# Optimization experiments

Measured on AMD Instinct MI355X. Metric: run time of the kernel, lower is better.

## Reference

```python
import jax, jax.numpy as jnp
import numpy as np

B, U, L, H, M = 4, 16, 128, 768, 256   # docs, utterances/doc, tokens/utt, hidden, mentions/doc
HID = 150                               # Score MLP hidden dim
N_CLUSTERS = 32


def setup_inputs() -> dict:
    key = jax.random.key(0)
    ks = jax.random.split(key, 8)
    hidden = jax.random.normal(ks[0], (B, U, L, H), jnp.float32)

    rng = np.random.default_rng(0)
    span_utt = rng.integers(0, U, (B, M))
    span_start = rng.integers(0, L - 8, (B, M))
    span_end = span_start + rng.integers(1, 9, (B, M))  # span length in [1, 8]

    # coreference labels: label[i, j] = 1 iff j is a true antecedent (j < i, same cluster);
    # if mention i has no antecedent, label[i, i] = 1 (the epsilon / new-entity slot).
    clusters = rng.integers(0, N_CLUSTERS, (B, M))
    same = clusters[:, :, None] == clusters[:, None, :]
    ant = same & np.tril(np.ones((M, M), bool), -1)
    labels = ant.astype(np.float32)
    diag = np.arange(M)
    labels[:, diag, diag] = (~ant.any(-1)).astype(np.float32)

    scale = 0.02
    W1 = jax.random.normal(ks[1], (3 * H, HID), jnp.float32) * scale
    W2 = jax.random.normal(ks[2], (HID, HID), jnp.float32) * scale
    W3 = jax.random.normal(ks[3], (HID, 1), jnp.float32) * scale
    return {
        "hidden": hidden,
        "span_utt": jnp.asarray(span_utt, jnp.int32),
        "span_start": jnp.asarray(span_start, jnp.int32),
        "span_end": jnp.asarray(span_end, jnp.int32),
        "labels": jnp.asarray(labels),
        "W1": W1, "b1": jnp.zeros((HID,), jnp.float32),
        "W2": W2, "b2": jnp.zeros((HID,), jnp.float32),
        "W3": W3, "b3": jnp.zeros((1,), jnp.float32),
    }


def reference(hidden, span_utt, span_start, span_end, labels, W1, b1, W2, b2, W3, b3):
    # ---- span mean-pooling (EntityEncoder, aggr='mean') ----
    pos = jnp.arange(L)
    mask = (pos[None, None, :] >= span_start[..., None]) & (pos[None, None, :] < span_end[..., None])
    w = mask.astype(hidden.dtype) / (span_end - span_start)[..., None].astype(hidden.dtype)  # [B,M,L]
    gathered = jnp.take_along_axis(hidden, span_utt[:, :, None, None], axis=1)  # [B,M,L,H]
    pooled = jnp.einsum('bml,bmlh->bmh', w, gathered)  # [B,M,H]

    # ---- pairwise antecedent scoring (PairScorer / Score MLP, dropout=eval) ----
    ii, jj = np.tril_indices(M, -1)  # static pair indices, P = M(M-1)/2
    # concat(i_g, j_g, i_g*j_g) @ W1  ==  i_g@W1a + j_g@W1b + (i_g*j_g)@W1c
    W1a, W1b, W1c = W1[:H], W1[H:2 * H], W1[2 * H:]
    hi = pooled @ W1a   # [B,M,HID]
    hj = pooled @ W1b   # [B,M,HID]
    prod = pooled[:, ii] * pooled[:, jj]                    # [B,P,H]
    h1 = jax.nn.relu(hi[:, ii] + hj[:, jj] + prod @ W1c + b1)
    h2 = jax.nn.relu(h1 @ W2 + b2)
    s = (h2 @ W3 + b3)[..., 0]  # [B,P]

    # ---- per-mention ragged softmax, padded to [M, M] with -1000 ----
    # row i has logits s_ij for j<i plus epsilon=0 at j=i (diagonal of zeros matrix)
    logits = jnp.zeros((B, M, M), hidden.dtype).at[:, ii, jj].set(s)
    valid = jnp.tril(jnp.ones((M, M), bool))
    probs = jax.nn.softmax(jnp.where(valid, logits, -1e30), axis=-1)
    probs = jnp.where(valid, probs, jnp.asarray(-1000.0, hidden.dtype))

    # ---- compute_loss ----
    eps = 1e-8
    prob_sum = jnp.sum(jnp.clip(probs * labels, eps, 1.0 - eps), axis=-1)  # [B,M]
    loss = -jnp.sum(jnp.log(prob_sum))
    return loss
```

## Files before the change

kernel.cpp:

```cpp
#include <hip/hip_runtime.h>
#include <hip/hip_bf16.h>

#define B_ 4
#define U_ 16
#define L_ 128
#define H_ 768
#define M_ 256
#define HID_ 150

typedef _Float16 half8 __attribute__((ext_vector_type(8)));
typedef _Float16 half4t __attribute__((ext_vector_type(4)));
typedef float floatx4 __attribute__((ext_vector_type(4)));
typedef float floatx16 __attribute__((ext_vector_type(16)));

__device__ __forceinline__ void gl_lds16(const _Float16* g, _Float16* l)
{
    __builtin_amdgcn_global_load_lds(
        (const __attribute__((address_space(1))) unsigned int*)g,
        (__attribute__((address_space(3))) unsigned int*)l, 16, 0, 0);
}

__global__ __launch_bounds__(256) void prep_kernel(
    const float* __restrict__ W1, const float* __restrict__ W2,
    const float* __restrict__ b2, const float* __restrict__ W3,
    _Float16* __restrict__ W1cs, _Float16* __restrict__ W2s,
    _Float16* __restrict__ W1abs, float2* __restrict__ bw)
{
    int idx = blockIdx.x * 256 + threadIdx.x;
    if (blockIdx.x == 0 && threadIdx.x < 160) {
        int n = threadIdx.x;
        bw[n] = (n < HID_) ? make_float2(b2[n], W3[n]) : make_float2(0.f, 0.f);
    }
    if (idx < 122880) {
        int k = idx / 160, n = idx - k * 160;
        float v = (n < HID_) ? W1[(size_t)(2 * H_ + k) * HID_ + n] : 0.f;
        W1cs[(k >> 4) * 2560 + (n >> 5) * 512 +
             (((n & 31) | (((k >> 3) & 1) << 5)) << 3) + (k & 7)] = (_Float16)v;
        return;
    }
    idx -= 122880;
    if (idx < 25600) {
        int k = idx / 160, n = idx - k * 160;
        float v = (k < HID_ && n < HID_) ? W2[(size_t)k * HID_ + n] : 0.f;
        W2s[(k >> 4) * 2560 + (n >> 5) * 512 +
            (((n & 31) | (((k >> 3) & 1) << 5)) << 3) + (k & 7)] = (_Float16)v;
        return;
    }
    idx -= 25600;
    if (idx < 245760) {
        int k = idx / 320, n = idx - k * 320;
        float v = 0.f;
        if (n < HID_) v = W1[(size_t)k * HID_ + n];
        else if (n >= 160 && n < 160 + HID_) v = W1[(size_t)(H_ + k) * HID_ + (n - 160)];
        W1abs[(k >> 5) * 10240 + (n >> 4) * 512 +
              (((n & 15) | (((k >> 3) & 3) << 4)) << 3) + (k & 7)] = (_Float16)v;
    }
}

__global__ __launch_bounds__(256) void pool_kernel(
    const float* __restrict__ hidden, const int* __restrict__ sutt,
    const int* __restrict__ sstart, const int* __restrict__ send,
    _Float16* __restrict__ pooledh)
{
    const int bm = blockIdx.x * 4 + (threadIdx.x >> 6);
    const int lane = threadIdx.x & 63;
    const int b  = bm >> 8;
    const int u  = sutt[bm];
    const int st = sstart[bm];
    const int en = send[bm];
    const float inv = 1.0f / (float)(en - st);
    const float* src = hidden + ((size_t)(b * U_ + u) * L_) * H_ + lane * 12;
    float4 s[3];
    #pragma unroll
    for (int q = 0; q < 3; ++q) s[q] = make_float4(0.f, 0.f, 0.f, 0.f);
    for (int l = st; l < en; ++l) {
        const float* p = src + (size_t)l * H_;
        #pragma unroll
        for (int q = 0; q < 3; ++q) {
            float4 v = *(const float4*)(p + q * 4);
            s[q].x += v.x; s[q].y += v.y; s[q].z += v.z; s[q].w += v.w;
        }
    }
    _Float16* gp = pooledh + (size_t)bm * H_ + lane * 12;
    #pragma unroll
    for (int q = 0; q < 3; ++q) {
        half4t hv;
        hv[0] = (_Float16)(s[q].x * inv); hv[1] = (_Float16)(s[q].y * inv);
        hv[2] = (_Float16)(s[q].z * inv); hv[3] = (_Float16)(s[q].w * inv);
        *(half4t*)(gp + q * 4) = hv;
    }
}

__global__ __launch_bounds__(256) void hihj_kernel(
    const _Float16* __restrict__ pooledh, const float* __restrict__ b1,
    const _Float16* __restrict__ W1abs,
    float* __restrict__ hiF, float* __restrict__ hjT)
{
    __shared__ __align__(16) _Float16 spool[16 * 776];
    const int blk = blockIdx.x;
    const int tid = threadIdx.x;
    for (int e = tid; e < 16 * 96; e += 256) {
        int r = e / 96, c = e - r * 96;
        *(half8*)&spool[r * 776 + c * 8] =
            *(const half8*)&pooledh[(size_t)(blk * 16 + r) * H_ + c * 8];
    }
    __syncthreads();

    const int w = tid >> 6, lane = tid & 63;
    const int g = lane >> 4, l15 = lane & 15;
    floatx4 acc[5];
    #pragma unroll
    for (int u5 = 0; u5 < 5; ++u5) acc[u5] = (floatx4){0.f, 0.f, 0.f, 0.f};
    const _Float16* aB = &spool[l15 * 776 + g * 8];
    for (int kc = 0; kc < 24; ++kc) {
        half8 av = *(const half8*)(aB + kc * 32);
        #pragma unroll
        for (int u5 = 0; u5 < 5; ++u5) {
            const int u = w * 5 + u5;
            half8 bv = *(const half8*)(W1abs + (size_t)((kc * 20 + u) * 64 + lane) * 8);
            acc[u5] = __builtin_amdgcn_mfma_f32_16x16x32_f16(av, bv, acc[u5], 0, 0, 0);
        }
    }
    const int row0 = blk * 16 + g * 4;
    #pragma unroll
    for (int u5 = 0; u5 < 5; ++u5) {
        const int n = (w * 5 + u5) * 16 + l15;
        if (n < HID_) {
            float b1v = b1[n];
            #pragma unroll
            for (int r = 0; r < 4; ++r)
                hiF[(size_t)(row0 + r) * 160 + n] = acc[u5][r] + b1v;
        } else if (n >= 160 && n < 160 + HID_) {
            *(float4*)&hjT[(size_t)(n - 160) * 1024 + row0] =
                make_float4(acc[u5][0], acc[u5][1], acc[u5][2], acc[u5][3]);
        }
    }
}

__global__ __launch_bounds__(128, 2) void pair_mlp_kernel(
    const _Float16* __restrict__ pooledh,
    const float* __restrict__ hiF, const float* __restrict__ hjT,
    const _Float16* __restrict__ W1cs, const _Float16* __restrict__ W2s,
    const float2* __restrict__ bw, const float* __restrict__ b3,
    float* __restrict__ logits)
{
    __shared__ __align__(16) _Float16 smem[2 * 5440];

    int q = blockIdx.x;
    const int b = q / 576;
    int r = q - b * 576;
    int jt = 0;
    while (r >= 128 - 16 * jt) { r -= 128 - 16 * jt; ++jt; }
    const int p = 16 * jt + r;
    const int i0 = 2 * p, j0 = jt * 32;
    const int bm = b * M_;
    const int w = threadIdx.x >> 6;
    const int lane = threadIdx.x & 63;
    const int c31 = lane & 31;
    const int hw = lane >> 5;

    _Float16* Wb0 = smem;
    _Float16* Wb1 = smem + 5120;
    _Float16* h1w = smem + w * 5440;

    const _Float16* pjp = pooledh + (size_t)(bm + j0 + c31) * H_ + (hw << 3);
    const _Float16* pip = pooledh + (size_t)(bm + i0 + w) * H_ + (hw << 3);

    floatx16 acc1[5];
    #pragma unroll
    for (int t1 = 0; t1 < 5; ++t1)
        #pragma unroll
        for (int e = 0; e < 16; ++e) acc1[t1][e] = 0.f;

    {
        const _Float16* gW = W1cs + (size_t)(5 * w) * 512 + lane * 8;
        #pragma unroll
        for (int c = 0; c < 5; ++c)
            gl_lds16(gW + c * 512, Wb0 + (5 * w + c) * 512);
    }
    half8 Apj0 = *(const half8*)(pjp);
    half8 Apj1 = *(const half8*)(pjp + 16);
    half8 Ai0  = *(const half8*)(pip);
    half8 Ai1  = *(const half8*)(pip + 16);
    __syncthreads();

    for (int kc = 0; kc < 24; ++kc) {
        const _Float16* Wcur = (kc & 1) ? Wb1 : Wb0;
        _Float16*       Wnxt = (kc & 1) ? Wb0 : Wb1;
        half8 npj0, npj1, ni0, ni1;
        if (kc < 23) {
            const _Float16* gW = W1cs + (size_t)(kc + 1) * 5120 + (5 * w) * 512 + lane * 8;
            #pragma unroll
            for (int c = 0; c < 5; ++c)
                gl_lds16(gW + c * 512, Wnxt + (5 * w + c) * 512);
            const int kb = (kc + 1) * 32;
            npj0 = *(const half8*)(pjp + kb);
            npj1 = *(const half8*)(pjp + kb + 16);
            ni0  = *(const half8*)(pip + kb);
            ni1  = *(const half8*)(pip + kb + 16);
        }
        {
            half8 a = Ai0 * Apj0;
            #pragma unroll
            for (int t1 = 0; t1 < 5; ++t1) {
                half8 wf = *(const half8*)&Wcur[t1 * 512 + lane * 8];
                acc1[t1] = __builtin_amdgcn_mfma_f32_32x32x16_f16(wf, a, acc1[t1], 0, 0, 0);
            }
        }
        {
            half8 a = Ai1 * Apj1;
            #pragma unroll
            for (int t1 = 0; t1 < 5; ++t1) {
                half8 wf = *(const half8*)&Wcur[(5 + t1) * 512 + lane * 8];
                acc1[t1] = __builtin_amdgcn_mfma_f32_32x32x16_f16(wf, a, acc1[t1], 0, 0, 0);
            }
        }
        if (kc < 23) { Apj0 = npj0; Apj1 = npj1; Ai0 = ni0; Ai1 = ni1; }
        __syncthreads();
    }

    const int jcol = bm + j0 + c31;
    #pragma unroll
    for (int t1 = 0; t1 < 5; ++t1) {
        #pragma unroll
        for (int qd = 0; qd < 4; ++qd) {
            const int n1 = t1 * 32 + 8 * qd + 4 * hw;
            float hj0 = hjT[(size_t)(n1 + 0) * 1024 + jcol];
            float hj1 = hjT[(size_t)(n1 + 1) * 1024 + jcol];
            float hj2 = hjT[(size_t)(n1 + 2) * 1024 + jcol];
            float hj3 = hjT[(size_t)(n1 + 3) * 1024 + jcol];
            float4 hiv = *(const float4*)&hiF[(size_t)(bm + i0 + w) * 160 + n1];
            half4t hv;
            hv[0] = (_Float16)fmaxf(acc1[t1][4 * qd + 0] + hiv.x + hj0, 0.f);
            hv[1] = (_Float16)fmaxf(acc1[t1][4 * qd + 1] + hiv.y + hj1, 0.f);
            hv[2] = (_Float16)fmaxf(acc1[t1][4 * qd + 2] + hiv.z + hj2, 0.f);
            hv[3] = (_Float16)fmaxf(acc1[t1][4 * qd + 3] + hiv.w + hj3, 0.f);
            *(half4t*)&h1w[c31 * 170 + n1] = hv;
        }
    }
    __syncthreads();

    const float b3v = b3[0];
    floatx16 acc2[5];
    #pragma unroll
    for (int t2 = 0; t2 < 5; ++t2)
        #pragma unroll
        for (int e = 0; e < 16; ++e) acc2[t2][e] = 0.f;

    half8 W2b[2][5], h1b[2];
    #pragma unroll
    for (int c = 0; c < 2; ++c) {
        const _Float16* wb = W2s + (size_t)(c * 5) * 512 + lane * 8;
        #pragma unroll
        for (int t2 = 0; t2 < 5; ++t2) W2b[c][t2] = *(const half8*)(wb + t2 * 512);
        h1b[c] = *(const half8*)&h1w[c31 * 170 + c * 16 + hw * 8];
    }
    for (int kc2 = 0; kc2 < 10; ++kc2) {
        const int cur = kc2 & 1;
        half8 nw[5], nh;
        if (kc2 < 8) {
            const _Float16* wb = W2s + (size_t)((kc2 + 2) * 5) * 512 + lane * 8;
            #pragma unroll
            for (int t2 = 0; t2 < 5; ++t2) nw[t2] = *(const half8*)(wb + t2 * 512);
            nh = *(const half8*)&h1w[c31 * 170 + (kc2 + 2) * 16 + hw * 8];
        }
        #pragma unroll
        for (int t2 = 0; t2 < 5; ++t2)
            acc2[t2] = __builtin_amdgcn_mfma_f32_32x32x16_f16(
                W2b[cur][t2], h1b[cur], acc2[t2], 0, 0, 0);
        if (kc2 < 8) {
            #pragma unroll
            for (int t2 = 0; t2 < 5; ++t2) W2b[cur][t2] = nw[t2];
            h1b[cur] = nh;
        }
    }

    float sown = 0.f;
    #pragma unroll
    for (int t2 = 0; t2 < 5; ++t2) {
        #pragma unroll
        for (int qd = 0; qd < 4; ++qd) {
            const int n2 = t2 * 32 + 8 * qd + 4 * hw;
            float4 bw01 = *(const float4*)&bw[n2];
            float4 bw23 = *(const float4*)&bw[n2 + 2];
            sown += fmaxf(acc2[t2][4 * qd + 0] + bw01.x, 0.f) * bw01.y;
            sown += fmaxf(acc2[t2][4 * qd + 1] + bw01.z, 0.f) * bw01.w;
            sown += fmaxf(acc2[t2][4 * qd + 2] + bw23.x, 0.f) * bw23.y;
            sown += fmaxf(acc2[t2][4 * qd + 3] + bw23.z, 0.f) * bw23.w;
        }
    }
    float s = sown + __shfl_xor(sown, 32);
    const int i = i0 + w;
    const int j = j0 + c31;
    if (lane < 32 && j < i)
        logits[(size_t)(bm + i) * M_ + j] = s + b3v;
}

__global__ __launch_bounds__(256) void loss_kernel(
    const float* __restrict__ logits, const float* __restrict__ labels,
    float* __restrict__ out)
{
    const int bm = blockIdx.x;
    const int i  = bm & (M_ - 1);
    const int j  = threadIdx.x;
    __shared__ float red[4];
    __shared__ float bcast;

    float val = (j < i) ? logits[(size_t)bm * M_ + j]
                        : ((j == i) ? 0.0f : -1e30f);

    float m = val;
    #pragma unroll
    for (int off = 32; off >= 1; off >>= 1) m = fmaxf(m, __shfl_down(m, off, 64));
    const int wave = j >> 6, lane = j & 63;
    if (lane == 0) red[wave] = m;
    __syncthreads();
    if (j == 0) bcast = fmaxf(fmaxf(red[0], red[1]), fmaxf(red[2], red[3]));
    __syncthreads();
    const float mm = bcast;

    float e = (j <= i) ? expf(val - mm) : 0.0f;
    float s = e;
    #pragma unroll
    for (int off = 32; off >= 1; off >>= 1) s += __shfl_down(s, off, 64);
    __syncthreads();
    if (lane == 0) red[wave] = s;
    __syncthreads();
    if (j == 0) bcast = red[0] + red[1] + red[2] + red[3];
    __syncthreads();
    const float ssum = bcast;

    float prob = (j <= i) ? (e / ssum) : -1000.0f;
    float lab = labels[(size_t)bm * M_ + j];
    float tv = prob * lab;
    tv = fminf(fmaxf(tv, 1e-8f), 1.0f - 1e-8f);
    float rs = tv;
    #pragma unroll
    for (int off = 32; off >= 1; off >>= 1) rs += __shfl_down(rs, off, 64);
    __syncthreads();
    if (lane == 0) red[wave] = rs;
    __syncthreads();
    if (j == 0) atomicAdd(out, -logf(red[0] + red[1] + red[2] + red[3]));
}

extern "C" void kernel_launch(void* const* d_in, const int* in_sizes, int n_in,
                              void* d_out, int out_size, void* d_ws, size_t ws_size,
                              hipStream_t stream)
{
    const float* hidden = (const float*)d_in[0];
    const int*   sutt   = (const int*)d_in[1];
    const int*   sstart = (const int*)d_in[2];
    const int*   send   = (const int*)d_in[3];
    const float* labels = (const float*)d_in[4];
    const float* W1     = (const float*)d_in[5];
    const float* b1     = (const float*)d_in[6];
    const float* W2     = (const float*)d_in[7];
    const float* b2     = (const float*)d_in[8];
    const float* W3     = (const float*)d_in[9];
    const float* b3     = (const float*)d_in[10];

    float* ws = (float*)d_ws;
    float*    hiF     = ws;
    float*    hjT     = ws + 163840;
    float*    logits  = ws + 327680;
    float2*   bw      = (float2*)(ws + 589824);
    _Float16* pooledh = (_Float16*)(ws + 590144);
    _Float16* W1cs    = (_Float16*)(ws + 983360);
    _Float16* W2s     = (_Float16*)(ws + 1106240);
    _Float16* W1abs   = (_Float16*)(ws + 1119040);
    float* out = (float*)d_out;

    hipMemsetAsync(d_out, 0, sizeof(float), stream);

    prep_kernel<<<dim3(1540), 256, 0, stream>>>(W1, W2, b2, W3,
                                                W1cs, W2s, W1abs, bw);
    pool_kernel<<<dim3(256), 256, 0, stream>>>(hidden, sutt, sstart, send, pooledh);
    hihj_kernel<<<dim3(64), 256, 0, stream>>>(pooledh, b1, W1abs, hiF, hjT);
    pair_mlp_kernel<<<dim3(576 * B_), 128, 0, stream>>>(pooledh, hiF, hjT,
                                                        W1cs, W2s, bw, b3, logits);
    loss_kernel<<<dim3(B_ * M_), 256, 0, stream>>>(logits, labels, out);
}
```

Measured before the change: 202.2 us.

## Use single-wave pair MLP blocks with register-prefetched W1c, fuse prep and pool

The pair MLP kernel goes from 2-wave blocks that staged W1c tiles through LDS with global_load_lds and a barrier per k-chunk to 1-wave blocks (twice as many). Each wave loads its W1c fragments straight from global into registers, double-buffered two chunks ahead, so the per-iteration __syncthreads goes away. Separately, the pooling kernel is merged into the weight-prep kernel as extra blocks, saving one launch. The trade-off is higher register pressure (20 half8 weight fragments plus the accumulators) and that each wave now reads the full W1c on its own instead of sharing it through LDS.

```diff
diff --git a/kernel.cpp b/kernel.cpp
--- a/kernel.cpp
+++ b/kernel.cpp
@@ -13,19 +13,45 @@
 typedef float floatx4 __attribute__((ext_vector_type(4)));
 typedef float floatx16 __attribute__((ext_vector_type(16)));
 
-__device__ __forceinline__ void gl_lds16(const _Float16* g, _Float16* l)
-{
-    __builtin_amdgcn_global_load_lds(
-        (const __attribute__((address_space(1))) unsigned int*)g,
-        (__attribute__((address_space(3))) unsigned int*)l, 16, 0, 0);
-}
-
-__global__ __launch_bounds__(256) void prep_kernel(
+__global__ __launch_bounds__(256) void prep_pool_kernel(
     const float* __restrict__ W1, const float* __restrict__ W2,
     const float* __restrict__ b2, const float* __restrict__ W3,
+    const float* __restrict__ hidden, const int* __restrict__ sutt,
+    const int* __restrict__ sstart, const int* __restrict__ send,
     _Float16* __restrict__ W1cs, _Float16* __restrict__ W2s,
-    _Float16* __restrict__ W1abs, float2* __restrict__ bw)
-{
+    _Float16* __restrict__ W1abs, float2* __restrict__ bw,
+    _Float16* __restrict__ pooledh)
+{
+    if (blockIdx.x >= 1540) {
+        const int bm = (blockIdx.x - 1540) * 4 + (threadIdx.x >> 6);
+        const int lane = threadIdx.x & 63;
+        const int b  = bm >> 8;
+        const int u  = sutt[bm];
+        const int st = sstart[bm];
+        const int en = send[bm];
+        const float inv = 1.0f / (float)(en - st);
+        const float* src = hidden + ((size_t)(b * U_ + u) * L_) * H_ + lane * 12;
+        float4 s[3];
+        #pragma unroll
+        for (int q = 0; q < 3; ++q) s[q] = make_float4(0.f, 0.f, 0.f, 0.f);
+        for (int l = st; l < en; ++l) {
+            const float* p = src + (size_t)l * H_;
+            #pragma unroll
+            for (int q = 0; q < 3; ++q) {
+                float4 v = *(const float4*)(p + q * 4);
+                s[q].x += v.x; s[q].y += v.y; s[q].z += v.z; s[q].w += v.w;
+            }
+        }
+        _Float16* gp = pooledh + (size_t)bm * H_ + lane * 12;
+        #pragma unroll
+        for (int q = 0; q < 3; ++q) {
+            half4t hv;
+            hv[0] = (_Float16)(s[q].x * inv); hv[1] = (_Float16)(s[q].y * inv);
+            hv[2] = (_Float16)(s[q].z * inv); hv[3] = (_Float16)(s[q].w * inv);
+            *(half4t*)(gp + q * 4) = hv;
+        }
+        return;
+    }
     int idx = blockIdx.x * 256 + threadIdx.x;
     if (blockIdx.x == 0 && threadIdx.x < 160) {
         int n = threadIdx.x;
@@ -57,40 +83,6 @@
     }
 }
 
-__global__ __launch_bounds__(256) void pool_kernel(
-    const float* __restrict__ hidden, const int* __restrict__ sutt,
-    const int* __restrict__ sstart, const int* __restrict__ send,
-    _Float16* __restrict__ pooledh)
-{
-    const int bm = blockIdx.x * 4 + (threadIdx.x >> 6);
-    const int lane = threadIdx.x & 63;
-    const int b  = bm >> 8;
-    const int u  = sutt[bm];
-    const int st = sstart[bm];
-    const int en = send[bm];
-    const float inv = 1.0f / (float)(en - st);
-    const float* src = hidden + ((size_t)(b * U_ + u) * L_) * H_ + lane * 12;
-    float4 s[3];
-    #pragma unroll
-    for (int q = 0; q < 3; ++q) s[q] = make_float4(0.f, 0.f, 0.f, 0.f);
-    for (int l = st; l < en; ++l) {
-        const float* p = src + (size_t)l * H_;
-        #pragma unroll
-        for (int q = 0; q < 3; ++q) {
-            float4 v = *(const float4*)(p + q * 4);
-            s[q].x += v.x; s[q].y += v.y; s[q].z += v.z; s[q].w += v.w;
-        }
-    }
-    _Float16* gp = pooledh + (size_t)bm * H_ + lane * 12;
-    #pragma unroll
-    for (int q = 0; q < 3; ++q) {
-        half4t hv;
-        hv[0] = (_Float16)(s[q].x * inv); hv[1] = (_Float16)(s[q].y * inv);
-        hv[2] = (_Float16)(s[q].z * inv); hv[3] = (_Float16)(s[q].w * inv);
-        *(half4t*)(gp + q * 4) = hv;
-    }
-}
-
 __global__ __launch_bounds__(256) void hihj_kernel(
     const _Float16* __restrict__ pooledh, const float* __restrict__ b1,
     const _Float16* __restrict__ W1abs,
@@ -137,34 +129,31 @@
     }
 }
 
-__global__ __launch_bounds__(128, 2) void pair_mlp_kernel(
+__global__ __launch_bounds__(64, 2) void pair_mlp_kernel(
     const _Float16* __restrict__ pooledh,
     const float* __restrict__ hiF, const float* __restrict__ hjT,
     const _Float16* __restrict__ W1cs, const _Float16* __restrict__ W2s,
     const float2* __restrict__ bw, const float* __restrict__ b3,
     float* __restrict__ logits)
 {
-    __shared__ __align__(16) _Float16 smem[2 * 5440];
+    __shared__ __align__(16) _Float16 h1L[32 * 170];
 
     int q = blockIdx.x;
-    const int b = q / 576;
-    int r = q - b * 576;
+    const int b = q / 1152;
+    int r2 = q - b * 1152;
+    const int t = r2 & 1;
+    int r = r2 >> 1;
     int jt = 0;
     while (r >= 128 - 16 * jt) { r -= 128 - 16 * jt; ++jt; }
     const int p = 16 * jt + r;
-    const int i0 = 2 * p, j0 = jt * 32;
+    const int i = 2 * p + t, j0 = jt * 32;
     const int bm = b * M_;
-    const int w = threadIdx.x >> 6;
     const int lane = threadIdx.x & 63;
     const int c31 = lane & 31;
     const int hw = lane >> 5;
 
-    _Float16* Wb0 = smem;
-    _Float16* Wb1 = smem + 5120;
-    _Float16* h1w = smem + w * 5440;
-
     const _Float16* pjp = pooledh + (size_t)(bm + j0 + c31) * H_ + (hw << 3);
-    const _Float16* pip = pooledh + (size_t)(bm + i0 + w) * H_ + (hw << 3);
+    const _Float16* pip = pooledh + (size_t)(bm + i) * H_ + (hw << 3);
 
     floatx16 acc1[5];
     #pragma unroll
@@ -172,51 +161,53 @@
         #pragma unroll
         for (int e = 0; e < 16; ++e) acc1[t1][e] = 0.f;
 
-    {
-        const _Float16* gW = W1cs + (size_t)(5 * w) * 512 + lane * 8;
-        #pragma unroll
-        for (int c = 0; c < 5; ++c)
-            gl_lds16(gW + c * 512, Wb0 + (5 * w + c) * 512);
-    }
-    half8 Apj0 = *(const half8*)(pjp);
-    half8 Apj1 = *(const half8*)(pjp + 16);
-    half8 Ai0  = *(const half8*)(pip);
-    half8 Ai1  = *(const half8*)(pip + 16);
-    __syncthreads();
+    half8 Apj0[2], Apj1[2], Ai0[2], Ai1[2];
+    half8 Wf[2][10];
+    #pragma unroll
+    for (int c = 0; c < 2; ++c) {
+        const int kb = c * 32;
+        Apj0[c] = *(const half8*)(pjp + kb);
+        Apj1[c] = *(const half8*)(pjp + kb + 16);
+        Ai0[c]  = *(const half8*)(pip + kb);
+        Ai1[c]  = *(const half8*)(pip + kb + 16);
+        const _Float16* wb = W1cs + (size_t)c * 5120 + lane * 8;
+        #pragma unroll
+        for (int u = 0; u < 10; ++u) Wf[c][u] = *(const half8*)(wb + u * 512);
+    }
 
     for (int kc = 0; kc < 24; ++kc) {
-        const _Float16* Wcur = (kc & 1) ? Wb1 : Wb0;
-        _Float16*       Wnxt = (kc & 1) ? Wb0 : Wb1;
-        half8 npj0, npj1, ni0, ni1;
-        if (kc < 23) {
-            const _Float16* gW = W1cs + (size_t)(kc + 1) * 5120 + (5 * w) * 512 + lane * 8;
-            #pragma unroll
-            for (int c = 0; c < 5; ++c)
-                gl_lds16(gW + c * 512, Wnxt + (5 * w + c) * 512);
-            const int kb = (kc + 1) * 32;
+        const int cur = kc & 1;
+        half8 npj0, npj1, ni0, ni1, nW[10];
+        if (kc < 22) {
+            const int kb = (kc + 2) * 32;
             npj0 = *(const half8*)(pjp + kb);
             npj1 = *(const half8*)(pjp + kb + 16);
             ni0  = *(const half8*)(pip + kb);
             ni1  = *(const half8*)(pip + kb + 16);
+            const _Float16* wb = W1cs + (size_t)(kc + 2) * 5120 + lane * 8;
+            #pragma unroll
+            for (int u = 0; u < 10; ++u) nW[u] = *(const half8*)(wb + u * 512);
         }
         {
-            half8 a = Ai0 * Apj0;
-            #pragma unroll
-            for (int t1 = 0; t1 < 5; ++t1) {
-                half8 wf = *(const half8*)&Wcur[t1 * 512 + lane * 8];
-                acc1[t1] = __builtin_amdgcn_mfma_f32_32x32x16_f16(wf, a, acc1[t1], 0, 0, 0);
-            }
+            half8 a = Ai0[cur] * Apj0[cur];
+            #pragma unroll
+            for (int t1 = 0; t1 < 5; ++t1)
+                acc1[t1] = __builtin_amdgcn_mfma_f32_32x32x16_f16(
+                    Wf[cur][t1], a, acc1[t1], 0, 0, 0);
         }
         {
-            half8 a = Ai1 * Apj1;
-            #pragma unroll
-            for (int t1 = 0; t1 < 5; ++t1) {
-                half8 wf = *(const half8*)&Wcur[(5 + t1) * 512 + lane * 8];
-                acc1[t1] = __builtin_amdgcn_mfma_f32_32x32x16_f16(wf, a, acc1[t1], 0, 0, 0);
-            }
-        }
-        if (kc < 23) { Apj0 = npj0; Apj1 = npj1; Ai0 = ni0; Ai1 = ni1; }
-        __syncthreads();
+            half8 a = Ai1[cur] * Apj1[cur];
+            #pragma unroll
+            for (int t1 = 0; t1 < 5; ++t1)
+                acc1[t1] = __builtin_amdgcn_mfma_f32_32x32x16_f16(
+                    Wf[cur][5 + t1], a, acc1[t1], 0, 0, 0);
+        }
+        if (kc < 22) {
+            Apj0[cur] = npj0; Apj1[cur] = npj1;
+            Ai0[cur] = ni0;   Ai1[cur] = ni1;
+            #pragma unroll
+            for (int u = 0; u < 10; ++u) Wf[cur][u] = nW[u];
+        }
     }
 
     const int jcol = bm + j0 + c31;
@@ -229,13 +220,13 @@
             float hj1 = hjT[(size_t)(n1 + 1) * 1024 + jcol];
             float hj2 = hjT[(size_t)(n1 + 2) * 1024 + jcol];
             float hj3 = hjT[(size_t)(n1 + 3) * 1024 + jcol];
-            float4 hiv = *(const float4*)&hiF[(size_t)(bm + i0 + w) * 160 + n1];
+            float4 hiv = *(const float4*)&hiF[(size_t)(bm + i) * 160 + n1];
             half4t hv;
             hv[0] = (_Float16)fmaxf(acc1[t1][4 * qd + 0] + hiv.x + hj0, 0.f);
             hv[1] = (_Float16)fmaxf(acc1[t1][4 * qd + 1] + hiv.y + hj1, 0.f);
             hv[2] = (_Float16)fmaxf(acc1[t1][4 * qd + 2] + hiv.z + hj2, 0.f);
             hv[3] = (_Float16)fmaxf(acc1[t1][4 * qd + 3] + hiv.w + hj3, 0.f);
-            *(half4t*)&h1w[c31 * 170 + n1] = hv;
+            *(half4t*)&h1L[c31 * 170 + n1] = hv;
         }
     }
     __syncthreads();
@@ -253,7 +244,7 @@
         const _Float16* wb = W2s + (size_t)(c * 5) * 512 + lane * 8;
         #pragma unroll
         for (int t2 = 0; t2 < 5; ++t2) W2b[c][t2] = *(const half8*)(wb + t2 * 512);
-        h1b[c] = *(const half8*)&h1w[c31 * 170 + c * 16 + hw * 8];
+        h1b[c] = *(const half8*)&h1L[c31 * 170 + c * 16 + hw * 8];
     }
     for (int kc2 = 0; kc2 < 10; ++kc2) {
         const int cur = kc2 & 1;
@@ -262,7 +253,7 @@
             const _Float16* wb = W2s + (size_t)((kc2 + 2) * 5) * 512 + lane * 8;
             #pragma unroll
             for (int t2 = 0; t2 < 5; ++t2) nw[t2] = *(const half8*)(wb + t2 * 512);
-            nh = *(const half8*)&h1w[c31 * 170 + (kc2 + 2) * 16 + hw * 8];
+            nh = *(const half8*)&h1L[c31 * 170 + (kc2 + 2) * 16 + hw * 8];
         }
         #pragma unroll
         for (int t2 = 0; t2 < 5; ++t2)
@@ -290,7 +281,6 @@
         }
     }
     float s = sown + __shfl_xor(sown, 32);
-    const int i = i0 + w;
     const int j = j0 + c31;
     if (lane < 32 && j < i)
         logits[(size_t)(bm + i) * M_ + j] = s + b3v;
@@ -372,11 +362,11 @@
 
     hipMemsetAsync(d_out, 0, sizeof(float), stream);
 
-    prep_kernel<<<dim3(1540), 256, 0, stream>>>(W1, W2, b2, W3,
-                                                W1cs, W2s, W1abs, bw);
-    pool_kernel<<<dim3(256), 256, 0, stream>>>(hidden, sutt, sstart, send, pooledh);
+    prep_pool_kernel<<<dim3(1796), 256, 0, stream>>>(
+        W1, W2, b2, W3, hidden, sutt, sstart, send,
+        W1cs, W2s, W1abs, bw, pooledh);
     hihj_kernel<<<dim3(64), 256, 0, stream>>>(pooledh, b1, W1abs, hiF, hjT);
-    pair_mlp_kernel<<<dim3(576 * B_), 128, 0, stream>>>(pooledh, hiF, hjT,
+    pair_mlp_kernel<<<dim3(1152 * B_), 64, 0, stream>>>(pooledh, hiF, hjT,
                                                         W1cs, W2s, bw, b3, logits);
     loss_kernel<<<dim3(B_ * M_), 256, 0, stream>>>(logits, labels, out);
 }
```

Result: slower. 234.7 us (+16.1%).

## Merge weight prep with span pooling and double K-chunk per W1c pipeline stage

Applied to the files above, without the earlier changes.

The weight-reformatting kernel and the span mean-pooling kernel become one launch: extra blocks past index 1540 do the pooling, which removes a launch and lets the two independent jobs overlap. In the pair MLP kernel, each double-buffered stage now loads two 32-wide K chunks of W1c (64 K values) into LDS instead of one. That halves the loop iterations and __syncthreads barriers from 24 to 12. The cost is twice the LDS footprint (about 40KB), which may reduce occupancy, plus more registers for the prefetched operands.

```diff
diff --git a/kernel.cpp b/kernel.cpp
--- a/kernel.cpp
+++ b/kernel.cpp
@@ -20,12 +20,45 @@
         (__attribute__((address_space(3))) unsigned int*)l, 16, 0, 0);
 }
 
-__global__ __launch_bounds__(256) void prep_kernel(
+__global__ __launch_bounds__(256) void prep_pool_kernel(
     const float* __restrict__ W1, const float* __restrict__ W2,
     const float* __restrict__ b2, const float* __restrict__ W3,
+    const float* __restrict__ hidden, const int* __restrict__ sutt,
+    const int* __restrict__ sstart, const int* __restrict__ send,
     _Float16* __restrict__ W1cs, _Float16* __restrict__ W2s,
-    _Float16* __restrict__ W1abs, float2* __restrict__ bw)
-{
+    _Float16* __restrict__ W1abs, float2* __restrict__ bw,
+    _Float16* __restrict__ pooledh)
+{
+    if (blockIdx.x >= 1540) {
+        const int bm = (blockIdx.x - 1540) * 4 + (threadIdx.x >> 6);
+        const int lane = threadIdx.x & 63;
+        const int b  = bm >> 8;
+        const int u  = sutt[bm];
+        const int st = sstart[bm];
+        const int en = send[bm];
+        const float inv = 1.0f / (float)(en - st);
+        const float* src = hidden + ((size_t)(b * U_ + u) * L_) * H_ + lane * 12;
+        float4 s[3];
+        #pragma unroll
+        for (int q = 0; q < 3; ++q) s[q] = make_float4(0.f, 0.f, 0.f, 0.f);
+        for (int l = st; l < en; ++l) {
+            const float* p = src + (size_t)l * H_;
+            #pragma unroll
+            for (int q = 0; q < 3; ++q) {
+                float4 v = *(const float4*)(p + q * 4);
+                s[q].x += v.x; s[q].y += v.y; s[q].z += v.z; s[q].w += v.w;
+            }
+        }
+        _Float16* gp = pooledh + (size_t)bm * H_ + lane * 12;
+        #pragma unroll
+        for (int q = 0; q < 3; ++q) {
+            half4t hv;
+            hv[0] = (_Float16)(s[q].x * inv); hv[1] = (_Float16)(s[q].y * inv);
+            hv[2] = (_Float16)(s[q].z * inv); hv[3] = (_Float16)(s[q].w * inv);
+            *(half4t*)(gp + q * 4) = hv;
+        }
+        return;
+    }
     int idx = blockIdx.x * 256 + threadIdx.x;
     if (blockIdx.x == 0 && threadIdx.x < 160) {
         int n = threadIdx.x;
@@ -57,40 +90,6 @@
     }
 }
 
-__global__ __launch_bounds__(256) void pool_kernel(
-    const float* __restrict__ hidden, const int* __restrict__ sutt,
-    const int* __restrict__ sstart, const int* __restrict__ send,
-    _Float16* __restrict__ pooledh)
-{
-    const int bm = blockIdx.x * 4 + (threadIdx.x >> 6);
-    const int lane = threadIdx.x & 63;
-    const int b  = bm >> 8;
-    const int u  = sutt[bm];
-    const int st = sstart[bm];
-    const int en = send[bm];
-    const float inv = 1.0f / (float)(en - st);
-    const float* src = hidden + ((size_t)(b * U_ + u) * L_) * H_ + lane * 12;
-    float4 s[3];
-    #pragma unroll
-    for (int q = 0; q < 3; ++q) s[q] = make_float4(0.f, 0.f, 0.f, 0.f);
-    for (int l = st; l < en; ++l) {
-        const float* p = src + (size_t)l * H_;
-        #pragma unroll
-        for (int q = 0; q < 3; ++q) {
-            float4 v = *(const float4*)(p + q * 4);
-            s[q].x += v.x; s[q].y += v.y; s[q].z += v.z; s[q].w += v.w;
-        }
-    }
-    _Float16* gp = pooledh + (size_t)bm * H_ + lane * 12;
-    #pragma unroll
-    for (int q = 0; q < 3; ++q) {
-        half4t hv;
-        hv[0] = (_Float16)(s[q].x * inv); hv[1] = (_Float16)(s[q].y * inv);
-        hv[2] = (_Float16)(s[q].z * inv); hv[3] = (_Float16)(s[q].w * inv);
-        *(half4t*)(gp + q * 4) = hv;
-    }
-}
-
 __global__ __launch_bounds__(256) void hihj_kernel(
     const _Float16* __restrict__ pooledh, const float* __restrict__ b1,
     const _Float16* __restrict__ W1abs,
@@ -144,7 +143,7 @@
     const float2* __restrict__ bw, const float* __restrict__ b3,
     float* __restrict__ logits)
 {
-    __shared__ __align__(16) _Float16 smem[2 * 5440];
+    __shared__ __align__(16) _Float16 smem[2 * 10240];
 
     int q = blockIdx.x;
     const int b = q / 576;
@@ -160,7 +159,7 @@
     const int hw = lane >> 5;
 
     _Float16* Wb0 = smem;
-    _Float16* Wb1 = smem + 5120;
+    _Float16* Wb1 = smem + 10240;
     _Float16* h1w = smem + w * 5440;
 
     const _Float16* pjp = pooledh + (size_t)(bm + j0 + c31) * H_ + (hw << 3);
@@ -175,47 +174,74 @@
     {
         const _Float16* gW = W1cs + (size_t)(5 * w) * 512 + lane * 8;
         #pragma unroll
-        for (int c = 0; c < 5; ++c)
-            gl_lds16(gW + c * 512, Wb0 + (5 * w + c) * 512);
-    }
-    half8 Apj0 = *(const half8*)(pjp);
-    half8 Apj1 = *(const half8*)(pjp + 16);
-    half8 Ai0  = *(const half8*)(pip);
-    half8 Ai1  = *(const half8*)(pip + 16);
-    __syncthreads();
-
-    for (int kc = 0; kc < 24; ++kc) {
-        const _Float16* Wcur = (kc & 1) ? Wb1 : Wb0;
-        _Float16*       Wnxt = (kc & 1) ? Wb0 : Wb1;
-        half8 npj0, npj1, ni0, ni1;
-        if (kc < 23) {
-            const _Float16* gW = W1cs + (size_t)(kc + 1) * 5120 + (5 * w) * 512 + lane * 8;
+        for (int cc = 0; cc < 2; ++cc)
             #pragma unroll
             for (int c = 0; c < 5; ++c)
-                gl_lds16(gW + c * 512, Wnxt + (5 * w + c) * 512);
-            const int kb = (kc + 1) * 32;
-            npj0 = *(const half8*)(pjp + kb);
-            npj1 = *(const half8*)(pjp + kb + 16);
-            ni0  = *(const half8*)(pip + kb);
-            ni1  = *(const half8*)(pip + kb + 16);
-        }
-        {
-            half8 a = Ai0 * Apj0;
-            #pragma unroll
-            for (int t1 = 0; t1 < 5; ++t1) {
-                half8 wf = *(const half8*)&Wcur[t1 * 512 + lane * 8];
-                acc1[t1] = __builtin_amdgcn_mfma_f32_32x32x16_f16(wf, a, acc1[t1], 0, 0, 0);
+                gl_lds16(gW + cc * 5120 + c * 512,
+                         Wb0 + cc * 5120 + (5 * w + c) * 512);
+    }
+    half8 Apj0[2], Apj1[2], Ai0[2], Ai1[2];
+    #pragma unroll
+    for (int cc = 0; cc < 2; ++cc) {
+        const int kb = cc * 32;
+        Apj0[cc] = *(const half8*)(pjp + kb);
+        Apj1[cc] = *(const half8*)(pjp + kb + 16);
+        Ai0[cc]  = *(const half8*)(pip + kb);
+        Ai1[cc]  = *(const half8*)(pip + kb + 16);
+    }
+    __syncthreads();
+
+    for (int kt = 0; kt < 12; ++kt) {
+        const _Float16* Wcur = (kt & 1) ? Wb1 : Wb0;
+        _Float16*       Wnxt = (kt & 1) ? Wb0 : Wb1;
+        half8 npj0[2], npj1[2], ni0[2], ni1[2];
+        if (kt < 11) {
+            const _Float16* gW = W1cs + (size_t)(kt + 1) * 10240
+                                 + (5 * w) * 512 + lane * 8;
+            #pragma unroll
+            for (int cc = 0; cc < 2; ++cc)
+                #pragma unroll
+                for (int c = 0; c < 5; ++c)
+                    gl_lds16(gW + cc * 5120 + c * 512,
+                             Wnxt + cc * 5120 + (5 * w + c) * 512);
+            const int kb = (kt + 1) * 64;
+            #pragma unroll
+            for (int cc = 0; cc < 2; ++cc) {
+                npj0[cc] = *(const half8*)(pjp + kb + cc * 32);
+                npj1[cc] = *(const half8*)(pjp + kb + cc * 32 + 16);
+                ni0[cc]  = *(const half8*)(pip + kb + cc * 32);
+                ni1[cc]  = *(const half8*)(pip + kb + cc * 32 + 16);
             }
         }
-        {
-            half8 a = Ai1 * Apj1;
-            #pragma unroll
-            for (int t1 = 0; t1 < 5; ++t1) {
-                half8 wf = *(const half8*)&Wcur[(5 + t1) * 512 + lane * 8];
-                acc1[t1] = __builtin_amdgcn_mfma_f32_32x32x16_f16(wf, a, acc1[t1], 0, 0, 0);
+        #pragma unroll
+        for (int cc = 0; cc < 2; ++cc) {
+            const _Float16* Wc = Wcur + cc * 5120;
+            {
+                half8 a = Ai0[cc] * Apj0[cc];
+                #pragma unroll
+                for (int t1 = 0; t1 < 5; ++t1) {
+                    half8 wf = *(const half8*)&Wc[t1 * 512 + lane * 8];
+                    acc1[t1] = __builtin_amdgcn_mfma_f32_32x32x16_f16(
+                        wf, a, acc1[t1], 0, 0, 0);
+                }
             }
-        }
-        if (kc < 23) { Apj0 = npj0; Apj1 = npj1; Ai0 = ni0; Ai1 = ni1; }
+            {
+                half8 a = Ai1[cc] * Apj1[cc];
+                #pragma unroll
+                for (int t1 = 0; t1 < 5; ++t1) {
+                    half8 wf = *(const half8*)&Wc[(5 + t1) * 512 + lane * 8];
+                    acc1[t1] = __builtin_amdgcn_mfma_f32_32x32x16_f16(
+                        wf, a, acc1[t1], 0, 0, 0);
+                }
+            }
+        }
+        if (kt < 11) {
+            #pragma unroll
+            for (int cc = 0; cc < 2; ++cc) {
+                Apj0[cc] = npj0[cc]; Apj1[cc] = npj1[cc];
+                Ai0[cc]  = ni0[cc];  Ai1[cc]  = ni1[cc];
+            }
+        }
         __syncthreads();
     }
 
@@ -372,9 +398,9 @@
 
     hipMemsetAsync(d_out, 0, sizeof(float), stream);
 
-    prep_kernel<<<dim3(1540), 256, 0, stream>>>(W1, W2, b2, W3,
-                                                W1cs, W2s, W1abs, bw);
-    pool_kernel<<<dim3(256), 256, 0, stream>>>(hidden, sutt, sstart, send, pooledh);
+    prep_pool_kernel<<<dim3(1796), 256, 0, stream>>>(
+        W1, W2, b2, W3, hidden, sutt, sstart, send,
+        W1cs, W2s, W1abs, bw, pooledh);
     hihj_kernel<<<dim3(64), 256, 0, stream>>>(pooledh, b1, W1abs, hiF, hjT);
     pair_mlp_kernel<<<dim3(576 * B_), 128, 0, stream>>>(pooledh, hiF, hjT,
                                                         W1cs, W2s, bw, b3, logits);
```

Result: slower. 206.3 us (+2.0%).

## Process four i-rows per pair block and merge prep with pooling kernel

Applied to the files above, without the earlier changes.

The pair MLP kernel now has each wave handle two i-rows instead of one. Every W1c tile staged in LDS and every pooled j-fragment load therefore feeds two MFMAs, which halves the grid and the per-row weight traffic. The weight-prep and span-pooling kernels are merged into one launch by giving pooling its own block range. The cost is twice the layer-1 accumulator registers per wave, which may lower occupancy under the 128,2 launch bounds, plus a serialized layer-2 pass per row.

```diff
diff --git a/kernel.cpp b/kernel.cpp
--- a/kernel.cpp
+++ b/kernel.cpp
@@ -20,12 +20,45 @@
         (__attribute__((address_space(3))) unsigned int*)l, 16, 0, 0);
 }
 
-__global__ __launch_bounds__(256) void prep_kernel(
+__global__ __launch_bounds__(256) void prep_pool_kernel(
     const float* __restrict__ W1, const float* __restrict__ W2,
     const float* __restrict__ b2, const float* __restrict__ W3,
+    const float* __restrict__ hidden, const int* __restrict__ sutt,
+    const int* __restrict__ sstart, const int* __restrict__ send,
     _Float16* __restrict__ W1cs, _Float16* __restrict__ W2s,
-    _Float16* __restrict__ W1abs, float2* __restrict__ bw)
-{
+    _Float16* __restrict__ W1abs, float2* __restrict__ bw,
+    _Float16* __restrict__ pooledh)
+{
+    if (blockIdx.x >= 1540) {
+        const int bm = (blockIdx.x - 1540) * 4 + (threadIdx.x >> 6);
+        const int lane = threadIdx.x & 63;
+        const int b  = bm >> 8;
+        const int u  = sutt[bm];
+        const int st = sstart[bm];
+        const int en = send[bm];
+        const float inv = 1.0f / (float)(en - st);
+        const float* src = hidden + ((size_t)(b * U_ + u) * L_) * H_ + lane * 12;
+        float4 s[3];
+        #pragma unroll
+        for (int q = 0; q < 3; ++q) s[q] = make_float4(0.f, 0.f, 0.f, 0.f);
+        for (int l = st; l < en; ++l) {
+            const float* p = src + (size_t)l * H_;
+            #pragma unroll
+            for (int q = 0; q < 3; ++q) {
+                float4 v = *(const float4*)(p + q * 4);
+                s[q].x += v.x; s[q].y += v.y; s[q].z += v.z; s[q].w += v.w;
+            }
+        }
+        _Float16* gp = pooledh + (size_t)bm * H_ + lane * 12;
+        #pragma unroll
+        for (int q = 0; q < 3; ++q) {
+            half4t hv;
+            hv[0] = (_Float16)(s[q].x * inv); hv[1] = (_Float16)(s[q].y * inv);
+            hv[2] = (_Float16)(s[q].z * inv); hv[3] = (_Float16)(s[q].w * inv);
+            *(half4t*)(gp + q * 4) = hv;
+        }
+        return;
+    }
     int idx = blockIdx.x * 256 + threadIdx.x;
     if (blockIdx.x == 0 && threadIdx.x < 160) {
         int n = threadIdx.x;
@@ -57,40 +90,6 @@
     }
 }
 
-__global__ __launch_bounds__(256) void pool_kernel(
-    const float* __restrict__ hidden, const int* __restrict__ sutt,
-    const int* __restrict__ sstart, const int* __restrict__ send,
-    _Float16* __restrict__ pooledh)
-{
-    const int bm = blockIdx.x * 4 + (threadIdx.x >> 6);
-    const int lane = threadIdx.x & 63;
-    const int b  = bm >> 8;
-    const int u  = sutt[bm];
-    const int st = sstart[bm];
-    const int en = send[bm];
-    const float inv = 1.0f / (float)(en - st);
-    const float* src = hidden + ((size_t)(b * U_ + u) * L_) * H_ + lane * 12;
-    float4 s[3];
-    #pragma unroll
-    for (int q = 0; q < 3; ++q) s[q] = make_float4(0.f, 0.f, 0.f, 0.f);
-    for (int l = st; l < en; ++l) {
-        const float* p = src + (size_t)l * H_;
-        #pragma unroll
-        for (int q = 0; q < 3; ++q) {
-            float4 v = *(const float4*)(p + q * 4);
-            s[q].x += v.x; s[q].y += v.y; s[q].z += v.z; s[q].w += v.w;
-        }
-    }
-    _Float16* gp = pooledh + (size_t)bm * H_ + lane * 12;
-    #pragma unroll
-    for (int q = 0; q < 3; ++q) {
-        half4t hv;
-        hv[0] = (_Float16)(s[q].x * inv); hv[1] = (_Float16)(s[q].y * inv);
-        hv[2] = (_Float16)(s[q].z * inv); hv[3] = (_Float16)(s[q].w * inv);
-        *(half4t*)(gp + q * 4) = hv;
-    }
-}
-
 __global__ __launch_bounds__(256) void hihj_kernel(
     const _Float16* __restrict__ pooledh, const float* __restrict__ b1,
     const _Float16* __restrict__ W1abs,
@@ -147,12 +146,12 @@
     __shared__ __align__(16) _Float16 smem[2 * 5440];
 
     int q = blockIdx.x;
-    const int b = q / 576;
-    int r = q - b * 576;
+    const int b = q / 288;
+    int r = q - b * 288;
     int jt = 0;
-    while (r >= 128 - 16 * jt) { r -= 128 - 16 * jt; ++jt; }
-    const int p = 16 * jt + r;
-    const int i0 = 2 * p, j0 = jt * 32;
+    while (r >= 64 - 8 * jt) { r -= 64 - 8 * jt; ++jt; }
+    const int p4 = 8 * jt + r;
+    const int i0 = 4 * p4, j0 = jt * 32;
     const int bm = b * M_;
     const int w = threadIdx.x >> 6;
     const int lane = threadIdx.x & 63;
@@ -163,14 +162,18 @@
     _Float16* Wb1 = smem + 5120;
     _Float16* h1w = smem + w * 5440;
 
-    const _Float16* pjp = pooledh + (size_t)(bm + j0 + c31) * H_ + (hw << 3);
-    const _Float16* pip = pooledh + (size_t)(bm + i0 + w) * H_ + (hw << 3);
-
-    floatx16 acc1[5];
-    #pragma unroll
-    for (int t1 = 0; t1 < 5; ++t1)
-        #pragma unroll
-        for (int e = 0; e < 16; ++e) acc1[t1][e] = 0.f;
+    const int ia = i0 + 2 * w;
+    const _Float16* pjp  = pooledh + (size_t)(bm + j0 + c31) * H_ + (hw << 3);
+    const _Float16* pipa = pooledh + (size_t)(bm + ia) * H_ + (hw << 3);
+    const _Float16* pipb = pooledh + (size_t)(bm + ia + 1) * H_ + (hw << 3);
+
+    floatx16 acc1[2][5];
+    #pragma unroll
+    for (int t = 0; t < 2; ++t)
+        #pragma unroll
+        for (int t1 = 0; t1 < 5; ++t1)
+            #pragma unroll
+            for (int e = 0; e < 16; ++e) acc1[t][t1][e] = 0.f;
 
     {
         const _Float16* gW = W1cs + (size_t)(5 * w) * 512 + lane * 8;
@@ -180,14 +183,16 @@
     }
     half8 Apj0 = *(const half8*)(pjp);
     half8 Apj1 = *(const half8*)(pjp + 16);
-    half8 Ai0  = *(const half8*)(pip);
-    half8 Ai1  = *(const half8*)(pip + 16);
+    half8 Aa0  = *(const half8*)(pipa);
+    half8 Aa1  = *(const half8*)(pipa + 16);
+    half8 Ab0  = *(const half8*)(pipb);
+    half8 Ab1  = *(const half8*)(pipb + 16);
     __syncthreads();
 
     for (int kc = 0; kc < 24; ++kc) {
         const _Float16* Wcur = (kc & 1) ? Wb1 : Wb0;
         _Float16*       Wnxt = (kc & 1) ? Wb0 : Wb1;
-        half8 npj0, npj1, ni0, ni1;
+        half8 npj0, npj1, na0, na1, nb0, nb1;
         if (kc < 23) {
             const _Float16* gW = W1cs + (size_t)(kc + 1) * 5120 + (5 * w) * 512 + lane * 8;
             #pragma unroll
@@ -196,104 +201,117 @@
             const int kb = (kc + 1) * 32;
             npj0 = *(const half8*)(pjp + kb);
             npj1 = *(const half8*)(pjp + kb + 16);
-            ni0  = *(const half8*)(pip + kb);
-            ni1  = *(const half8*)(pip + kb + 16);
+            na0  = *(const half8*)(pipa + kb);
+            na1  = *(const half8*)(pipa + kb + 16);
+            nb0  = *(const half8*)(pipb + kb);
+            nb1  = *(const half8*)(pipb + kb + 16);
         }
         {
-            half8 a = Ai0 * Apj0;
+            half8 a0 = Aa0 * Apj0;
+            half8 a1 = Ab0 * Apj0;
             #pragma unroll
             for (int t1 = 0; t1 < 5; ++t1) {
                 half8 wf = *(const half8*)&Wcur[t1 * 512 + lane * 8];
-                acc1[t1] = __builtin_amdgcn_mfma_f32_32x32x16_f16(wf, a, acc1[t1], 0, 0, 0);
+                acc1[0][t1] = __builtin_amdgcn_mfma_f32_32x32x16_f16(wf, a0, acc1[0][t1], 0, 0, 0);
+                acc1[1][t1] = __builtin_amdgcn_mfma_f32_32x32x16_f16(wf, a1, acc1[1][t1], 0, 0, 0);
             }
         }
         {
-            half8 a = Ai1 * Apj1;
+            half8 a0 = Aa1 * Apj1;
+            half8 a1 = Ab1 * Apj1;
             #pragma unroll
             for (int t1 = 0; t1 < 5; ++t1) {
                 half8 wf = *(const half8*)&Wcur[(5 + t1) * 512 + lane * 8];
-                acc1[t1] = __builtin_amdgcn_mfma_f32_32x32x16_f16(wf, a, acc1[t1], 0, 0, 0);
-            }
-        }
-        if (kc < 23) { Apj0 = npj0; Apj1 = npj1; Ai0 = ni0; Ai1 = ni1; }
+                acc1[0][t1] = __builtin_amdgcn_mfma_f32_32x32x16_f16(wf, a0, acc1[0][t1], 0, 0, 0);
+                acc1[1][t1] = __builtin_amdgcn_mfma_f32_32x32x16_f16(wf, a1, acc1[1][t1], 0, 0, 0);
+            }
+        }
+        if (kc < 23) {
+            Apj0 = npj0; Apj1 = npj1;
+            Aa0 = na0; Aa1 = na1; Ab0 = nb0; Ab1 = nb1;
+        }
         __syncthreads();
     }
 
+    const float b3v = b3[0];
     const int jcol = bm + j0 + c31;
     #pragma unroll
-    for (int t1 = 0; t1 < 5; ++t1) {
-        #pragma unroll
-        for (int qd = 0; qd < 4; ++qd) {
-            const int n1 = t1 * 32 + 8 * qd + 4 * hw;
-            float hj0 = hjT[(size_t)(n1 + 0) * 1024 + jcol];
-            float hj1 = hjT[(size_t)(n1 + 1) * 1024 + jcol];
-            float hj2 = hjT[(size_t)(n1 + 2) * 1024 + jcol];
-            float hj3 = hjT[(size_t)(n1 + 3) * 1024 + jcol];
-            float4 hiv = *(const float4*)&hiF[(size_t)(bm + i0 + w) * 160 + n1];
-            half4t hv;
-            hv[0] = (_Float16)fmaxf(acc1[t1][4 * qd + 0] + hiv.x + hj0, 0.f);
-            hv[1] = (_Float16)fmaxf(acc1[t1][4 * qd + 1] + hiv.y + hj1, 0.f);
-            hv[2] = (_Float16)fmaxf(acc1[t1][4 * qd + 2] + hiv.z + hj2, 0.f);
-            hv[3] = (_Float16)fmaxf(acc1[t1][4 * qd + 3] + hiv.w + hj3, 0.f);
-            *(half4t*)&h1w[c31 * 170 + n1] = hv;
-        }
-    }
-    __syncthreads();
-
-    const float b3v = b3[0];
-    floatx16 acc2[5];
-    #pragma unroll
-    for (int t2 = 0; t2 < 5; ++t2)
-        #pragma unroll
-        for (int e = 0; e < 16; ++e) acc2[t2][e] = 0.f;
-
-    half8 W2b[2][5], h1b[2];
-    #pragma unroll
-    for (int c = 0; c < 2; ++c) {
-        const _Float16* wb = W2s + (size_t)(c * 5) * 512 + lane * 8;
-        #pragma unroll
-        for (int t2 = 0; t2 < 5; ++t2) W2b[c][t2] = *(const half8*)(wb + t2 * 512);
-        h1b[c] = *(const half8*)&h1w[c31 * 170 + c * 16 + hw * 8];
-    }
-    for (int kc2 = 0; kc2 < 10; ++kc2) {
-        const int cur = kc2 & 1;
-        half8 nw[5], nh;
-        if (kc2 < 8) {
-            const _Float16* wb = W2s + (size_t)((kc2 + 2) * 5) * 512 + lane * 8;
-            #pragma unroll
-            for (int t2 = 0; t2 < 5; ++t2) nw[t2] = *(const half8*)(wb + t2 * 512);
-            nh = *(const half8*)&h1w[c31 * 170 + (kc2 + 2) * 16 + hw * 8];
-        }
+    for (int t = 0; t < 2; ++t) {
+        const int irow = ia + t;
+        __syncthreads();
+        #pragma unroll
+        for (int t1 = 0; t1 < 5; ++t1) {
+            #pragma unroll
+            for (int qd = 0; qd < 4; ++qd) {
+                const int n1 = t1 * 32 + 8 * qd + 4 * hw;
+                float hj0 = hjT[(size_t)(n1 + 0) * 1024 + jcol];
+                float hj1 = hjT[(size_t)(n1 + 1) * 1024 + jcol];
+                float hj2 = hjT[(size_t)(n1 + 2) * 1024 + jcol];
+                float hj3 = hjT[(size_t)(n1 + 3) * 1024 + jcol];
+                float4 hiv = *(const float4*)&hiF[(size_t)(bm + irow) * 160 + n1];
+                half4t hv;
+                hv[0] = (_Float16)fmaxf(acc1[t][t1][4 * qd + 0] + hiv.x + hj0, 0.f);
+                hv[1] = (_Float16)fmaxf(acc1[t][t1][4 * qd + 1] + hiv.y + hj1, 0.f);
+                hv[2] = (_Float16)fmaxf(acc1[t][t1][4 * qd + 2] + hiv.z + hj2, 0.f);
+                hv[3] = (_Float16)fmaxf(acc1[t][t1][4 * qd + 3] + hiv.w + hj3, 0.f);
+                *(half4t*)&h1w[c31 * 170 + n1] = hv;
+            }
+        }
+        __syncthreads();
+
+        floatx16 acc2[5];
         #pragma unroll
         for (int t2 = 0; t2 < 5; ++t2)
-            acc2[t2] = __builtin_amdgcn_mfma_f32_32x32x16_f16(
-                W2b[cur][t2], h1b[cur], acc2[t2], 0, 0, 0);
-        if (kc2 < 8) {
-            #pragma unroll
-            for (int t2 = 0; t2 < 5; ++t2) W2b[cur][t2] = nw[t2];
-            h1b[cur] = nh;
-        }
-    }
-
-    float sown = 0.f;
-    #pragma unroll
-    for (int t2 = 0; t2 < 5; ++t2) {
-        #pragma unroll
-        for (int qd = 0; qd < 4; ++qd) {
-            const int n2 = t2 * 32 + 8 * qd + 4 * hw;
-            float4 bw01 = *(const float4*)&bw[n2];
-            float4 bw23 = *(const float4*)&bw[n2 + 2];
-            sown += fmaxf(acc2[t2][4 * qd + 0] + bw01.x, 0.f) * bw01.y;
-            sown += fmaxf(acc2[t2][4 * qd + 1] + bw01.z, 0.f) * bw01.w;
-            sown += fmaxf(acc2[t2][4 * qd + 2] + bw23.x, 0.f) * bw23.y;
-            sown += fmaxf(acc2[t2][4 * qd + 3] + bw23.z, 0.f) * bw23.w;
-        }
-    }
-    float s = sown + __shfl_xor(sown, 32);
-    const int i = i0 + w;
-    const int j = j0 + c31;
-    if (lane < 32 && j < i)
-        logits[(size_t)(bm + i) * M_ + j] = s + b3v;
+            #pragma unroll
+            for (int e = 0; e < 16; ++e) acc2[t2][e] = 0.f;
+
+        half8 W2b[2][5], h1b[2];
+        #pragma unroll
+        for (int c = 0; c < 2; ++c) {
+            const _Float16* wb = W2s + (size_t)(c * 5) * 512 + lane * 8;
+            #pragma unroll
+            for (int t2 = 0; t2 < 5; ++t2) W2b[c][t2] = *(const half8*)(wb + t2 * 512);
+            h1b[c] = *(const half8*)&h1w[c31 * 170 + c * 16 + hw * 8];
+        }
+        for (int kc2 = 0; kc2 < 10; ++kc2) {
+            const int cur = kc2 & 1;
+            half8 nw[5], nh;
+            if (kc2 < 8) {
+                const _Float16* wb = W2s + (size_t)((kc2 + 2) * 5) * 512 + lane * 8;
+                #pragma unroll
+                for (int t2 = 0; t2 < 5; ++t2) nw[t2] = *(const half8*)(wb + t2 * 512);
+                nh = *(const half8*)&h1w[c31 * 170 + (kc2 + 2) * 16 + hw * 8];
+            }
+            #pragma unroll
+            for (int t2 = 0; t2 < 5; ++t2)
+                acc2[t2] = __builtin_amdgcn_mfma_f32_32x32x16_f16(
+                    W2b[cur][t2], h1b[cur], acc2[t2], 0, 0, 0);
+            if (kc2 < 8) {
+                #pragma unroll
+                for (int t2 = 0; t2 < 5; ++t2) W2b[cur][t2] = nw[t2];
+                h1b[cur] = nh;
+            }
+        }
+
+        float sown = 0.f;
+        #pragma unroll
+        for (int t2 = 0; t2 < 5; ++t2) {
+            #pragma unroll
+            for (int qd = 0; qd < 4; ++qd) {
+                const int n2 = t2 * 32 + 8 * qd + 4 * hw;
+                float4 bw01 = *(const float4*)&bw[n2];
+                float4 bw23 = *(const float4*)&bw[n2 + 2];
+                sown += fmaxf(acc2[t2][4 * qd + 0] + bw01.x, 0.f) * bw01.y;
+                sown += fmaxf(acc2[t2][4 * qd + 1] + bw01.z, 0.f) * bw01.w;
+                sown += fmaxf(acc2[t2][4 * qd + 2] + bw23.x, 0.f) * bw23.y;
+                sown += fmaxf(acc2[t2][4 * qd + 3] + bw23.z, 0.f) * bw23.w;
+            }
+        }
+        float s = sown + __shfl_xor(sown, 32);
+        const int j = j0 + c31;
+        if (lane < 32 && j < irow)
+            logits[(size_t)(bm + irow) * M_ + j] = s + b3v;
+    }
 }
 
 __global__ __launch_bounds__(256) void loss_kernel(
@@ -372,11 +390,11 @@
 
     hipMemsetAsync(d_out, 0, sizeof(float), stream);
 
-    prep_kernel<<<dim3(1540), 256, 0, stream>>>(W1, W2, b2, W3,
-                                                W1cs, W2s, W1abs, bw);
-    pool_kernel<<<dim3(256), 256, 0, stream>>>(hidden, sutt, sstart, send, pooledh);
+    prep_pool_kernel<<<dim3(1796), 256, 0, stream>>>(
+        W1, W2, b2, W3, hidden, sutt, sstart, send,
+        W1cs, W2s, W1abs, bw, pooledh);
     hihj_kernel<<<dim3(64), 256, 0, stream>>>(pooledh, b1, W1abs, hiF, hjT);
-    pair_mlp_kernel<<<dim3(576 * B_), 128, 0, stream>>>(pooledh, hiF, hjT,
+    pair_mlp_kernel<<<dim3(288 * B_), 128, 0, stream>>>(pooledh, hiF, hjT,
                                                         W1cs, W2s, bw, b3, logits);
     loss_kernel<<<dim3(B_ * M_), 256, 0, stream>>>(logits, labels, out);
 }
```

Measured after the change: 250.8 us. 24.1% more time.
